# Kernel optimization log

Measured on AMD Instinct MI355X. Metric: run time of the kernel, lower is better.

Reference implementation:

```python
import jax, jax.numpy as jnp
import numpy as np

RATIO = 0.9375  # config.ratio


def setup_inputs() -> dict:
    key = jax.random.key(0)
    x = jax.random.normal(key, (4096, 8192), dtype=jnp.float32)
    return {"x": x}


def reference(x):
    # recall_window(x, ratio, dim=-1, keepdim=False)
    # For each row: sort, then find the minimum-length window covering
    # target = int(ratio * N) consecutive sorted values; return (left, right).
    N = x.shape[-1]
    target = int(RATIO * N)
    s = jnp.sort(x, axis=-1)                       # [R, N]
    # window_length[i] = s[i + target - 1] - s[i], for i in [0, N - target]
    lengths = s[:, target - 1:] - s[:, : N - target + 1]   # [R, N - target + 1]
    idx = jnp.argmin(lengths, axis=-1)             # first min, matches '<' in loop
    left = jnp.take_along_axis(s, idx[:, None], axis=-1)[:, 0]
    right = jnp.take_along_axis(s, (idx + target - 1)[:, None], axis=-1)[:, 0]
    return left, right
```

## Files before the change

kernel.cpp:

```cpp
#include <hip/hip_runtime.h>
#include <stdint.h>

#define ROWS   4096
#define NCOL   8192
#define TARGET 7680
#define NW     (NCOL - TARGET + 1)
#define NT     256
#define VPT    (NCOL / NT)
#define NB     2048
#define NSB    1024
#define SCAP   3072
#define MAXS   (SCAP / NT)

struct Smem {
    uint32_t hist[NB];
    float    sorted[SCAP];
    uint32_t wsum[8];
    uint32_t res[4];
    uint32_t aux[2];
    float    fmin[4], fmax[4];
    float    rv[4];
    int      ri[4];
};

__device__ __forceinline__ int bin1f(float v, float mn, float s) {
    int b = (int)((v - mn) * s);
    return b < 0 ? 0 : (b > NB - 1 ? NB - 1 : b);
}
__device__ __forceinline__ int sbin_bot(float v, float mn, float sb) {
    int b = (int)((v - mn) * sb);
    return b < 0 ? 0 : (b > NSB - 1 ? NSB - 1 : b);
}
__device__ __forceinline__ int sbin_top(float v, float mx, float st) {
    int b = (int)((mx - v) * st);
    b = b < 0 ? 0 : (b > NSB - 1 ? NSB - 1 : b);
    return (NSB - 1) - b;
}

__device__ void locate2(Smem& sm, uint32_t ka, uint32_t kb, int tid) {
    const int lane = tid & 63, wid = tid >> 6;
    const int base = tid * 8;
    uint32_t h[8], s0 = 0;
    #pragma unroll
    for (int j = 0; j < 8; j++) { h[j] = sm.hist[base + j]; s0 += h[j]; }
    uint32_t sc = s0;
    #pragma unroll
    for (int off = 1; off < 64; off <<= 1) {
        uint32_t n = __shfl_up(sc, off, 64);
        if (lane >= off) sc += n;
    }
    if (lane == 63) sm.wsum[wid] = sc;
    __syncthreads();
    uint32_t woff = 0;
    for (int w = 0; w < wid; w++) woff += sm.wsum[w];
    uint32_t incl = sc + woff, excl = incl - s0;
    if (ka >= excl && ka < incl) {
        uint32_t c = excl; bool done = false;
        #pragma unroll
        for (int j = 0; j < 8; j++) {
            if (!done) {
                if (ka < c + h[j]) { sm.res[0] = (uint32_t)(base + j); done = true; }
                else c += h[j];
            }
        }
    }
    if (kb >= excl && kb < incl) {
        uint32_t c = excl; bool done = false;
        #pragma unroll
        for (int j = 0; j < 8; j++) {
            if (!done) {
                if (kb < c + h[j]) { sm.res[2] = (uint32_t)(base + j); done = true; }
                else c += h[j];
            }
        }
    }
    __syncthreads();
}

__device__ void scan_offsets(Smem& sm, int tid) {
    const int lane = tid & 63, wid = tid >> 6;
    const int base = tid * 8;
    uint32_t h[8], s0 = 0;
    #pragma unroll
    for (int j = 0; j < 8; j++) { h[j] = sm.hist[base + j]; s0 += h[j]; }
    uint32_t sc = s0;
    #pragma unroll
    for (int off = 1; off < 64; off <<= 1) {
        uint32_t n = __shfl_up(sc, off, 64);
        if (lane >= off) sc += n;
    }
    if (lane == 63) sm.wsum[wid] = sc;
    __syncthreads();
    uint32_t woff = 0;
    for (int w = 0; w < wid; w++) woff += sm.wsum[w];
    uint32_t run = sc - s0 + woff;
    if (tid == (NSB / 8)) sm.aux[0] = run;
    #pragma unroll
    for (int j = 0; j < 8; j++) { sm.hist[base + j] = run; run += h[j]; }
    if (tid == NT - 1) sm.aux[1] = run;
    __syncthreads();
}

__global__ __launch_bounds__(NT, 4)
void recall_window_kernel(const float* __restrict__ x, float* __restrict__ out) {
    __shared__ Smem sm;
    const int tid = threadIdx.x;
    const int row = blockIdx.x;
    const int lane = tid & 63, wid = tid >> 6;

    float v[VPT];
    const float4* xv = (const float4*)(x + (size_t)row * NCOL);
    #pragma unroll
    for (int j = 0; j < VPT / 4; j++) {
        float4 t = xv[tid + j * NT];
        v[4 * j + 0] = t.x; v[4 * j + 1] = t.y;
        v[4 * j + 2] = t.z; v[4 * j + 3] = t.w;
    }

    float mn = v[0], mx = v[0];
    #pragma unroll
    for (int j = 1; j < VPT; j++) { mn = fminf(mn, v[j]); mx = fmaxf(mx, v[j]); }
    #pragma unroll
    for (int off = 32; off > 0; off >>= 1) {
        mn = fminf(mn, __shfl_down(mn, off, 64));
        mx = fmaxf(mx, __shfl_down(mx, off, 64));
    }
    if (lane == 0) { sm.fmin[wid] = mn; sm.fmax[wid] = mx; }
    #pragma unroll
    for (int j = 0; j < 8; j++) sm.hist[tid + j * NT] = 0;
    __syncthreads();
    mn = fminf(fminf(sm.fmin[0], sm.fmin[1]), fminf(sm.fmin[2], sm.fmin[3]));
    mx = fmaxf(fmaxf(sm.fmax[0], sm.fmax[1]), fmaxf(sm.fmax[2], sm.fmax[3]));

    if (!(mx > mn)) {
        if (tid == 0) { out[row] = mn; out[ROWS + row] = mn; }
        return;
    }
    const float scale1 = (float)NB / (mx - mn);

    #pragma unroll
    for (int j = 0; j < VPT; j++) atomicAdd(&sm.hist[bin1f(v[j], mn, scale1)], 1u);
    __syncthreads();
    locate2(sm, NW - 1, TARGET - 1, tid);
    const int B_lo = (int)sm.res[0];
    const int B_hi = (int)sm.res[2];

    #pragma unroll
    for (int j = 0; j < 8; j++) sm.hist[tid + j * NT] = 0;
    __syncthreads();
    const float scale_b = (float)NSB * scale1 / (float)(B_lo + 1);
    const float scale_t = (float)NSB * scale1 / (float)(NB - B_hi);
    #pragma unroll
    for (int j = 0; j < VPT; j++) {
        float val = v[j];
        int b1 = bin1f(val, mn, scale1);
        if (b1 <= B_lo)      atomicAdd(&sm.hist[sbin_bot(val, mn, scale_b)], 1u);
        else if (b1 >= B_hi) atomicAdd(&sm.hist[NSB + sbin_top(val, mx, scale_t)], 1u);
    }
    __syncthreads();
    scan_offsets(sm, tid);
    const uint32_t cb  = sm.aux[0];
    uint32_t tot = sm.aux[1]; if (tot > SCAP) tot = SCAP;

    #pragma unroll
    for (int j = 0; j < VPT; j++) {
        float val = v[j];
        int b1 = bin1f(val, mn, scale1);
        int gb = -1;
        if (b1 <= B_lo)      gb = sbin_bot(val, mn, scale_b);
        else if (b1 >= B_hi) gb = NSB + sbin_top(val, mx, scale_t);
        if (gb >= 0) {
            uint32_t pos = atomicAdd(&sm.hist[gb], 1u);
            if (pos < SCAP) sm.sorted[pos] = val;
        }
    }
    __syncthreads();

    int   tgt[MAXS];
    float fvv[MAXS];
    #pragma unroll
    for (int it = 0; it < MAXS; it++) {
        int s = tid + it * NT;
        tgt[it] = -1;
        if (s < (int)tot) {
            float vv = sm.sorted[s];
            int gb = (s < (int)cb) ? sbin_bot(vv, mn, scale_b)
                                   : (NSB + sbin_top(vv, mx, scale_t));
            uint32_t start = (gb == 0) ? 0u : sm.hist[gb - 1];
            uint32_t end   = sm.hist[gb];
            if (end > SCAP) end = SCAP;
            uint32_t r = 0;
            if (end - start > 1) {
                for (uint32_t q = start; q < end; q++) {
                    float u = sm.sorted[q];
                    r += (u < vv) || (u == vv && (int)q < s);
                }
            }
            tgt[it] = (int)(start + r);
            fvv[it] = vv;
        }
    }
    __syncthreads();
    #pragma unroll
    for (int it = 0; it < MAXS; it++)
        if (tgt[it] >= 0) sm.sorted[tgt[it]] = fvv[it];
    __syncthreads();


    const int topstart = (int)tot - NW;
    float lbest = __int_as_float(0x7F800000);
    int   lidx  = 0x7FFFFFFF;
    for (int i = tid; i < NW; i += NT) {
        float len = sm.sorted[topstart + i] - sm.sorted[i];
        if (len < lbest) { lbest = len; lidx = i; }
    }
    #pragma unroll
    for (int off = 32; off > 0; off >>= 1) {
        float v2 = __shfl_down(lbest, off, 64);
        int   i2 = __shfl_down(lidx,  off, 64);
        if (v2 < lbest || (v2 == lbest && i2 < lidx)) { lbest = v2; lidx = i2; }
    }
    if (lane == 0) { sm.rv[wid] = lbest; sm.ri[wid] = lidx; }
    __syncthreads();
    if (tid == 0) {
        float bv = sm.rv[0]; int bi = sm.ri[0];
        #pragma unroll
        for (int w = 1; w < 4; w++) {
            float v2 = sm.rv[w]; int i2 = sm.ri[w];
            if (v2 < bv || (v2 == bv && i2 < bi)) { bv = v2; bi = i2; }
        }
        out[row]        = sm.sorted[bi];
        out[ROWS + row] = sm.sorted[topstart + bi];
    }
}

extern "C" void kernel_launch(void* const* d_in, const int* in_sizes, int n_in,
                              void* d_out, int out_size, void* d_ws, size_t ws_size,
                              hipStream_t stream) {
    const float* x = (const float*)d_in[0];
    float* out = (float*)d_out;
    recall_window_kernel<<<ROWS, NT, 0, stream>>>(x, out);
}
```

Measured before the change: 223.0 us.

## Double block size, cache sub-bin indices, sort buckets in place by insertion sort

Doubles the threads per row-block to 512, so each thread holds 16 values and owns 4 histogram bins, read and written as uint4. Sub-bin indices from the counting pass are packed into 16-bit registers and reused in the scatter pass instead of being recomputed. The per-element rank-by-counting sort within buckets is replaced by a per-bucket insertion sort done by the thread that owns the bucket, so rank buffers and the extra scatter are no longer needed. The insertion sort is serial within a bucket and can diverge across threads when bucket sizes are uneven, and the larger block changes register and occupancy pressure.

Measured after the change: 258.9 us. 1.16x slower.

```diff
diff --git a/kernel.cpp b/kernel.cpp
--- a/kernel.cpp
+++ b/kernel.cpp
@@ -5,22 +5,23 @@
 #define NCOL   8192
 #define TARGET 7680
 #define NW     (NCOL - TARGET + 1)
-#define NT     256
+#define NT     512
 #define VPT    (NCOL / NT)
+#define NWAVE  (NT / 64)
 #define NB     2048
+#define BPT    (NB / NT)
 #define NSB    1024
 #define SCAP   3072
-#define MAXS   (SCAP / NT)
-
-struct Smem {
+
+struct __align__(16) Smem {
     uint32_t hist[NB];
     float    sorted[SCAP];
-    uint32_t wsum[8];
+    uint32_t wsum[NWAVE];
     uint32_t res[4];
     uint32_t aux[2];
-    float    fmin[4], fmax[4];
-    float    rv[4];
-    int      ri[4];
+    float    fmin[NWAVE], fmax[NWAVE];
+    float    rv[NWAVE];
+    int      ri[NWAVE];
 };
 
 __device__ __forceinline__ int bin1f(float v, float mn, float s) {
@@ -39,10 +40,9 @@
 
 __device__ void locate2(Smem& sm, uint32_t ka, uint32_t kb, int tid) {
     const int lane = tid & 63, wid = tid >> 6;
-    const int base = tid * 8;
-    uint32_t h[8], s0 = 0;
-    #pragma unroll
-    for (int j = 0; j < 8; j++) { h[j] = sm.hist[base + j]; s0 += h[j]; }
+    uint4 hv = ((const uint4*)sm.hist)[tid];
+    uint32_t h[4] = {hv.x, hv.y, hv.z, hv.w};
+    uint32_t s0 = h[0] + h[1] + h[2] + h[3];
     uint32_t sc = s0;
     #pragma unroll
     for (int off = 1; off < 64; off <<= 1) {
@@ -57,9 +57,9 @@
     if (ka >= excl && ka < incl) {
         uint32_t c = excl; bool done = false;
         #pragma unroll
-        for (int j = 0; j < 8; j++) {
+        for (int j = 0; j < 4; j++) {
             if (!done) {
-                if (ka < c + h[j]) { sm.res[0] = (uint32_t)(base + j); done = true; }
+                if (ka < c + h[j]) { sm.res[0] = (uint32_t)(tid * 4 + j); done = true; }
                 else c += h[j];
             }
         }
@@ -67,9 +67,9 @@
     if (kb >= excl && kb < incl) {
         uint32_t c = excl; bool done = false;
         #pragma unroll
-        for (int j = 0; j < 8; j++) {
+        for (int j = 0; j < 4; j++) {
             if (!done) {
-                if (kb < c + h[j]) { sm.res[2] = (uint32_t)(base + j); done = true; }
+                if (kb < c + h[j]) { sm.res[2] = (uint32_t)(tid * 4 + j); done = true; }
                 else c += h[j];
             }
         }
@@ -79,10 +79,9 @@
 
 __device__ void scan_offsets(Smem& sm, int tid) {
     const int lane = tid & 63, wid = tid >> 6;
-    const int base = tid * 8;
-    uint32_t h[8], s0 = 0;
-    #pragma unroll
-    for (int j = 0; j < 8; j++) { h[j] = sm.hist[base + j]; s0 += h[j]; }
+    uint4 hv = ((const uint4*)sm.hist)[tid];
+    uint32_t h[4] = {hv.x, hv.y, hv.z, hv.w};
+    uint32_t s0 = h[0] + h[1] + h[2] + h[3];
     uint32_t sc = s0;
     #pragma unroll
     for (int off = 1; off < 64; off <<= 1) {
@@ -93,15 +92,18 @@
     __syncthreads();
     uint32_t woff = 0;
     for (int w = 0; w < wid; w++) woff += sm.wsum[w];
-    uint32_t run = sc - s0 + woff;
-    if (tid == (NSB / 8)) sm.aux[0] = run;
-    #pragma unroll
-    for (int j = 0; j < 8; j++) { sm.hist[base + j] = run; run += h[j]; }
+    uint32_t run = (sc - s0) + woff;
+    uint4 ov;
+    ov.x = run; run += h[0];
+    ov.y = run; run += h[1];
+    ov.z = run; run += h[2];
+    ov.w = run; run += h[3];
+    ((uint4*)sm.hist)[tid] = ov;
     if (tid == NT - 1) sm.aux[1] = run;
     __syncthreads();
 }
 
-__global__ __launch_bounds__(NT, 4)
+__global__ __launch_bounds__(NT, 8)
 void recall_window_kernel(const float* __restrict__ x, float* __restrict__ out) {
     __shared__ Smem sm;
     const int tid = threadIdx.x;
@@ -126,11 +128,17 @@
         mx = fmaxf(mx, __shfl_down(mx, off, 64));
     }
     if (lane == 0) { sm.fmin[wid] = mn; sm.fmax[wid] = mx; }
-    #pragma unroll
-    for (int j = 0; j < 8; j++) sm.hist[tid + j * NT] = 0;
-    __syncthreads();
-    mn = fminf(fminf(sm.fmin[0], sm.fmin[1]), fminf(sm.fmin[2], sm.fmin[3]));
-    mx = fmaxf(fmaxf(sm.fmax[0], sm.fmax[1]), fmaxf(sm.fmax[2], sm.fmax[3]));
+    {
+        uint4 z; z.x = z.y = z.z = z.w = 0u;
+        ((uint4*)sm.hist)[tid] = z;
+    }
+    __syncthreads();
+    mn = sm.fmin[0]; mx = sm.fmax[0];
+    #pragma unroll
+    for (int w = 1; w < NWAVE; w++) {
+        mn = fminf(mn, sm.fmin[w]);
+        mx = fmaxf(mx, sm.fmax[w]);
+    }
 
     if (!(mx > mn)) {
         if (tid == 0) { out[row] = mn; out[ROWS + row] = mn; }
@@ -144,66 +152,68 @@
     locate2(sm, NW - 1, TARGET - 1, tid);
     const int B_lo = (int)sm.res[0];
     const int B_hi = (int)sm.res[2];
-
-    #pragma unroll
-    for (int j = 0; j < 8; j++) sm.hist[tid + j * NT] = 0;
-    __syncthreads();
+    {
+        uint4 z; z.x = z.y = z.z = z.w = 0u;
+        ((uint4*)sm.hist)[tid] = z;
+    }
+    __syncthreads();
+
     const float scale_b = (float)NSB * scale1 / (float)(B_lo + 1);
     const float scale_t = (float)NSB * scale1 / (float)(NB - B_hi);
-    #pragma unroll
-    for (int j = 0; j < VPT; j++) {
-        float val = v[j];
-        int b1 = bin1f(val, mn, scale1);
-        if (b1 <= B_lo)      atomicAdd(&sm.hist[sbin_bot(val, mn, scale_b)], 1u);
-        else if (b1 >= B_hi) atomicAdd(&sm.hist[NSB + sbin_top(val, mx, scale_t)], 1u);
+    uint32_t gbp[VPT / 2];
+    #pragma unroll
+    for (int jp = 0; jp < VPT / 2; jp++) {
+        uint32_t enc = 0;
+        #pragma unroll
+        for (int h = 0; h < 2; h++) {
+            float val = v[2 * jp + h];
+            int b1 = bin1f(val, mn, scale1);
+            int gb = -1;
+            if (b1 <= B_lo)      gb = sbin_bot(val, mn, scale_b);
+            else if (b1 >= B_hi) gb = NSB + sbin_top(val, mx, scale_t);
+            uint32_t g16 = (gb >= 0) ? (uint32_t)(gb + 1) : 0u;
+            if (gb >= 0) atomicAdd(&sm.hist[gb], 1u);
+            enc |= g16 << (16 * h);
+        }
+        gbp[jp] = enc;
     }
     __syncthreads();
     scan_offsets(sm, tid);
-    const uint32_t cb  = sm.aux[0];
     uint32_t tot = sm.aux[1]; if (tot > SCAP) tot = SCAP;
 
     #pragma unroll
-    for (int j = 0; j < VPT; j++) {
-        float val = v[j];
-        int b1 = bin1f(val, mn, scale1);
-        int gb = -1;
-        if (b1 <= B_lo)      gb = sbin_bot(val, mn, scale_b);
-        else if (b1 >= B_hi) gb = NSB + sbin_top(val, mx, scale_t);
-        if (gb >= 0) {
-            uint32_t pos = atomicAdd(&sm.hist[gb], 1u);
-            if (pos < SCAP) sm.sorted[pos] = val;
-        }
-    }
-    __syncthreads();
-
-    int   tgt[MAXS];
-    float fvv[MAXS];
-    #pragma unroll
-    for (int it = 0; it < MAXS; it++) {
-        int s = tid + it * NT;
-        tgt[it] = -1;
-        if (s < (int)tot) {
-            float vv = sm.sorted[s];
-            int gb = (s < (int)cb) ? sbin_bot(vv, mn, scale_b)
-                                   : (NSB + sbin_top(vv, mx, scale_t));
-            uint32_t start = (gb == 0) ? 0u : sm.hist[gb - 1];
-            uint32_t end   = sm.hist[gb];
-            if (end > SCAP) end = SCAP;
-            uint32_t r = 0;
-            if (end - start > 1) {
-                for (uint32_t q = start; q < end; q++) {
-                    float u = sm.sorted[q];
-                    r += (u < vv) || (u == vv && (int)q < s);
+    for (int jp = 0; jp < VPT / 2; jp++) {
+        uint32_t enc = gbp[jp];
+        #pragma unroll
+        for (int h = 0; h < 2; h++) {
+            uint32_t g16 = (enc >> (16 * h)) & 0xFFFFu;
+            if (g16) {
+                uint32_t pos = atomicAdd(&sm.hist[g16 - 1], 1u);
+                if (pos < SCAP) sm.sorted[pos] = v[2 * jp + h];
+            }
+        }
+    }
+    __syncthreads();
+
+    #pragma unroll
+    for (int j = 0; j < BPT; j++) {
+        int b = tid * BPT + j;
+        uint32_t start = (b == 0) ? 0u : sm.hist[b - 1];
+        uint32_t end   = sm.hist[b];
+        if (start > SCAP) start = SCAP;
+        if (end   > SCAP) end   = SCAP;
+        if (end > start + 1) {
+            for (uint32_t i = start + 1; i < end; i++) {
+                float key = sm.sorted[i];
+                int q = (int)i - 1;
+                while (q >= (int)start && sm.sorted[q] > key) {
+                    sm.sorted[q + 1] = sm.sorted[q];
+                    q--;
                 }
-            }
-            tgt[it] = (int)(start + r);
-            fvv[it] = vv;
-        }
-    }
-    __syncthreads();
-    #pragma unroll
-    for (int it = 0; it < MAXS; it++)
-        if (tgt[it] >= 0) sm.sorted[tgt[it]] = fvv[it];
+                sm.sorted[q + 1] = key;
+            }
+        }
+    }
     __syncthreads();
 
 
@@ -225,7 +235,7 @@
     if (tid == 0) {
         float bv = sm.rv[0]; int bi = sm.ri[0];
         #pragma unroll
-        for (int w = 1; w < 4; w++) {
+        for (int w = 1; w < NWAVE; w++) {
             float v2 = sm.rv[w]; int i2 = sm.ri[w];
             if (v2 < bv || (v2 == bv && i2 < bi)) { bv = v2; bi = i2; }
         }
```
